# Performance work log

Measured on AMD Instinct MI355X. Metric: run time of the kernel, lower is better.

The kernel has to match this reference:

```python
import jax, jax.numpy as jnp
import numpy as np

B, Q, K, A, H, C, O = 32, 512, 512, 256, 8, 32, 256  # batch, queries, keys, channels, heads, head_dim, out_dim


def setup_inputs() -> dict:
    key = jax.random.key(0)
    ks = jax.random.split(key, 12)
    s = 0.02
    return {
        "q_data": jax.random.normal(ks[0], (B, Q, A), jnp.float32),
        "m_data": jax.random.normal(ks[1], (B, K, A), jnp.float32),
        "bias": jax.random.normal(ks[2], (B, 1, 1, K), jnp.float32),
        "nonbatched_bias": jax.random.normal(ks[3], (H, Q, K), jnp.float32),
        "batched_bias": jax.random.normal(ks[4], (B, H, Q, K), jnp.float32),
        "query_w": jax.random.normal(ks[5], (A, H, C), jnp.float32) * s,
        "key_w": jax.random.normal(ks[6], (A, H, C), jnp.float32) * s,
        "value_w": jax.random.normal(ks[7], (A, H, C), jnp.float32) * s,
        "gating_w": jax.random.normal(ks[8], (A, H, C), jnp.float32) * s,
        "gating_b": jnp.ones((H, C), jnp.float32),
        "output_w": jax.random.normal(ks[9], (H, C, O), jnp.float32) * s,
        "output_b": jnp.zeros((O,), jnp.float32),
    }


def reference(q_data, m_data, bias, nonbatched_bias, batched_bias,
              query_w, key_w, value_w, gating_w, gating_b, output_w, output_b):
    key_scale = query_w.shape[-1] ** -0.5
    q = jnp.einsum('bqa,ahc->bqhc', q_data, query_w) * key_scale
    k = jnp.einsum('bka,ahc->bkhc', m_data, key_w)
    v = jnp.einsum('bka,ahc->bkhc', m_data, value_w)
    logits = jnp.einsum('bqhc,bkhc->bhqk', q, k) + bias
    logits = logits + nonbatched_bias[None] + batched_bias
    weights = jax.nn.softmax(logits, axis=-1)
    weighted_avg = jnp.einsum('bhqk,bkhc->bqhc', weights, v)
    gate = jax.nn.sigmoid(jnp.einsum('bqc,chv->bqhv', q_data, gating_w) + gating_b)
    weighted_avg = weighted_avg * gate
    return jnp.einsum('bqhc,hco->bqo', weighted_avg, output_w) + output_b
```

## Files before the change

kernel.cpp:

```cpp
#include <hip/hip_runtime.h>
#include <cstdint>
#include <cstddef>


typedef __attribute__((ext_vector_type(8))) short short8;
typedef __attribute__((ext_vector_type(4))) float f32x4;
typedef __attribute__((ext_vector_type(4))) unsigned int u32x4;
typedef __attribute__((ext_vector_type(2))) unsigned int u32x2;

#define DEVFN static __device__ __forceinline__
#define L2E 1.4426950408889634f

DEVFN float b2f(unsigned int bits16) {
  return __builtin_bit_cast(float, bits16 << 16);
}
DEVFN unsigned int pack2(float a, float b) {
  unsigned int r;
  asm("v_cvt_pk_bf16_f32 %0, %1, %2" : "=v"(r) : "v"(a), "v"(b));
  return r;
}
DEVFN f32x4 mfma16(short8 a, short8 b, f32x4 c) {
  return __builtin_amdgcn_mfma_f32_16x16x32_bf16(a, b, c, 0, 0, 0);
}
#define GLOAD_LDS16(gp, lp)                                        \
  __builtin_amdgcn_global_load_lds(                                \
      (const __attribute__((address_space(1))) void*)(gp),         \
      (__attribute__((address_space(3))) void*)(lp), 16, 0, 0)

__global__ __launch_bounds__(256) void wtrans_kernel(
    const float* __restrict__ qw, const float* __restrict__ kw,
    const float* __restrict__ vw, const float* __restrict__ gw,
    const float* __restrict__ ow,
    unsigned short* __restrict__ wtq, unsigned short* __restrict__ wtk,
    unsigned short* __restrict__ wtv, unsigned short* __restrict__ wtg,
    unsigned short* __restrict__ wt3)
{
  const int matid = blockIdx.x >> 4;
  const int tile  = blockIdx.x & 15;
  const float* src = (matid == 0) ? qw : (matid == 1) ? kw : (matid == 2) ? vw
                   : (matid == 3) ? gw : ow;
  unsigned short* dst = (matid == 0) ? wtq : (matid == 1) ? wtk : (matid == 2) ? wtv
                      : (matid == 3) ? wtg : wt3;
  const int tr = (tile >> 2) * 64, tc = (tile & 3) * 64;
  __shared__ unsigned short T[64 * 72];
  const int t = threadIdx.x;
  {
    const int row = t >> 2, cb = (t & 3) * 16;
#pragma unroll
    for (int ii = 0; ii < 4; ++ii) {
      f32x4 v = *(const f32x4*)&src[(size_t)(tr + row) * 256 + tc + cb + ii * 4];
      u32x2 p; p.x = pack2(v.x, v.y); p.y = pack2(v.z, v.w);
      *(u32x2*)&T[row * 72 + cb + ii * 4] = p;
    }
  }
  __syncthreads();
  {
    const int c0 = t >> 2, rb = (t & 3) * 16;
    unsigned short vals[16];
#pragma unroll
    for (int m = 0; m < 16; ++m) vals[m] = T[(rb + m) * 72 + c0];
    u32x4 s0, s1;
    s0.x = (unsigned)vals[0]  | ((unsigned)vals[1]  << 16);
    s0.y = (unsigned)vals[2]  | ((unsigned)vals[3]  << 16);
    s0.z = (unsigned)vals[4]  | ((unsigned)vals[5]  << 16);
    s0.w = (unsigned)vals[6]  | ((unsigned)vals[7]  << 16);
    s1.x = (unsigned)vals[8]  | ((unsigned)vals[9]  << 16);
    s1.y = (unsigned)vals[10] | ((unsigned)vals[11] << 16);
    s1.z = (unsigned)vals[12] | ((unsigned)vals[13] << 16);
    s1.w = (unsigned)vals[14] | ((unsigned)vals[15] << 16);
    unsigned short* dp = &dst[(size_t)(tc + c0) * 256 + tr + rb];
    *(u32x4*)dp = s0;
    *(u32x4*)(dp + 8) = s1;
  }
}

__global__ __launch_bounds__(512, 4) void proj_kernel(
    const float* __restrict__ q_data, const float* __restrict__ m_data,
    const unsigned short* __restrict__ wtq, const unsigned short* __restrict__ wtk,
    const unsigned short* __restrict__ wtv, const unsigned short* __restrict__ wtg,
    const float* __restrict__ gating_b,
    unsigned short* __restrict__ qp, unsigned short* __restrict__ kp,
    unsigned short* __restrict__ vp, unsigned short* __restrict__ gate)
{
  const int bid = blockIdx.x;
  const bool mside = bid >= 256;
  const int r0 = (mside ? bid - 256 : bid) * 64;
  const float* inp = mside ? m_data : q_data;
  __shared__ unsigned short Alds[64 * 264];
  __shared__ unsigned short Wlds[2][256 * 40];
  const int t = threadIdx.x;
  const int lane = t & 63, wave = t >> 6;
  const int l15 = lane & 15, g = lane >> 4;
  const int stripe = wave & 3, nhalf = wave >> 2;

  {
    const int row = t >> 3, cb = (t & 7) * 32;
    const float* ip = &inp[(size_t)(r0 + row) * 256 + cb];
#pragma unroll
    for (int i = 0; i < 4; ++i) {
      f32x4 a0 = *(const f32x4*)&ip[i * 8];
      f32x4 a1 = *(const f32x4*)&ip[i * 8 + 4];
      u32x4 pk;
      pk.x = pack2(a0.x, a0.y); pk.y = pack2(a0.z, a0.w);
      pk.z = pack2(a1.x, a1.y); pk.w = pack2(a1.z, a1.w);
      *(u32x4*)&Alds[row * 264 + cb + i * 8] = pk;
    }
  }

  const unsigned short* wt0 = mside ? wtk : wtq;
  const unsigned short* wt1 = mside ? wtv : wtg;
  const int wrow = t & 255, whalf = t >> 8;

  {
    const u32x4* wsrc = (const u32x4*)&wt0[(size_t)wrow * 256 + whalf * 16];
    u32x4 a = wsrc[0], b = wsrc[1];
    *(u32x4*)&Wlds[0][wrow * 40 + whalf * 16 + 0] = a;
    *(u32x4*)&Wlds[0][wrow * 40 + whalf * 16 + 8] = b;
  }

  f32x4 acc[8];
#pragma unroll
  for (int j = 0; j < 8; ++j) acc[j] = f32x4{0.f, 0.f, 0.f, 0.f};

  const int arow = (stripe * 16 + l15) * 264 + 8 * g;
  const int grow = r0 + stripe * 16 + l15;
  const int ob = grow >> 9, oq = grow & 511;

#pragma unroll
  for (int s = 0; s < 16; ++s) {
    const int p = s & 1;
    __syncthreads();
    u32x4 nw0, nw1;
    if (s < 15) {
      const unsigned short* wt = (s + 1 < 8) ? wt0 : wt1;
      const u32x4* wsrc =
          (const u32x4*)&wt[(size_t)wrow * 256 + ((s + 1) & 7) * 32 + whalf * 16];
      nw0 = wsrc[0]; nw1 = wsrc[1];
    }
    const int ks = s & 7;
    short8 bf = __builtin_bit_cast(short8, *(const u32x4*)&Alds[arow + ks * 32]);
#pragma unroll
    for (int j = 0; j < 8; ++j) {
      short8 wf = __builtin_bit_cast(short8,
          *(const u32x4*)&Wlds[p][((nhalf * 8 + j) * 16 + l15) * 40 + 8 * g]);
      acc[j] = mfma16(wf, bf, acc[j]);
    }
    if (s < 15) {
      *(u32x4*)&Wlds[p ^ 1][wrow * 40 + whalf * 16 + 0] = nw0;
      *(u32x4*)&Wlds[p ^ 1][wrow * 40 + whalf * 16 + 8] = nw1;
    }
    if (s == 7 || s == 15) {
      const int oi = s >> 3;
      const float QS = 0.17677669529663687f * 1.4426950408889634f;
#pragma unroll
      for (int j = 0; j < 8; ++j) {
        const int n0 = (nhalf * 8 + j) * 16 + 4 * g;
        const int h = n0 >> 5, c0 = n0 & 31;
        const size_t idx = ((size_t)(ob * 8 + h) * 512 + oq) * 32 + c0;
        f32x4 v = acc[j];
        if (!mside) {
          if (oi == 0) {
            u32x2 st;
            st.x = pack2(v.x * QS, v.y * QS);
            st.y = pack2(v.z * QS, v.w * QS);
            *(u32x2*)&qp[idx] = st;
          } else {
            f32x4 gb = *(const f32x4*)&gating_b[n0];
            f32x4 gv;
            gv.x = 1.0f / (1.0f + exp2f(-(v.x + gb.x) * L2E));
            gv.y = 1.0f / (1.0f + exp2f(-(v.y + gb.y) * L2E));
            gv.z = 1.0f / (1.0f + exp2f(-(v.z + gb.z) * L2E));
            gv.w = 1.0f / (1.0f + exp2f(-(v.w + gb.w) * L2E));
            u32x2 st;
            st.x = pack2(gv.x, gv.y); st.y = pack2(gv.z, gv.w);
            *(u32x2*)&gate[idx] = st;
          }
        } else {
          u32x2 st;
          st.x = pack2(v.x, v.y); st.y = pack2(v.z, v.w);
          if (oi == 0) *(u32x2*)&kp[idx] = st;
          else         *(u32x2*)&vp[idx] = st;
        }
        acc[j] = f32x4{0.f, 0.f, 0.f, 0.f};
      }
    }
  }
}

__global__ __launch_bounds__(512, 2) void attn_kernel(
    const unsigned short* __restrict__ qp, const unsigned short* __restrict__ kp,
    const unsigned short* __restrict__ vp,
    const float* __restrict__ bias, const float* __restrict__ nbias,
    const float* __restrict__ bbias,
    unsigned short* __restrict__ wa)
{
  const int bid = blockIdx.x;
  const int h = bid & 7;
  const int qh = (bid >> 3) & 1;
  const int b = bid >> 4;
  const int bh = b * 8 + h;
  const int t = threadIdx.x;
  const int lane = t & 63, wave = t >> 6;
  const int l15 = lane & 15, g = lane >> 4;

  __shared__ unsigned short Klds[512 * 40];
  __shared__ unsigned short Vt[32 * 520];
  __shared__ float Bb[2][8192];
  __shared__ float Bk[512];

  {
    const int row = t;
    const u32x4* ks = (const u32x4*)&kp[((size_t)bh * 512 + row) * 32];
    u32x4 k0 = ks[0], k1 = ks[1], k2 = ks[2], k3 = ks[3];
    *(u32x4*)&Klds[row * 40 + 0]  = k0;
    *(u32x4*)&Klds[row * 40 + 8]  = k1;
    *(u32x4*)&Klds[row * 40 + 16] = k2;
    *(u32x4*)&Klds[row * 40 + 24] = k3;
    const u32x4* vs = (const u32x4*)&vp[((size_t)bh * 512 + row) * 32];
#pragma unroll
    for (int cc = 0; cc < 4; ++cc) {
      u32x4 vv = vs[cc];
      unsigned int dw0 = vv.x, dw1 = vv.y, dw2 = vv.z, dw3 = vv.w;
      const int c = cc * 8;
      Vt[(c + 0) * 520 + row] = (unsigned short)(dw0 & 0xffff);
      Vt[(c + 1) * 520 + row] = (unsigned short)(dw0 >> 16);
      Vt[(c + 2) * 520 + row] = (unsigned short)(dw1 & 0xffff);
      Vt[(c + 3) * 520 + row] = (unsigned short)(dw1 >> 16);
      Vt[(c + 4) * 520 + row] = (unsigned short)(dw2 & 0xffff);
      Vt[(c + 5) * 520 + row] = (unsigned short)(dw2 >> 16);
      Vt[(c + 6) * 520 + row] = (unsigned short)(dw3 & 0xffff);
      Vt[(c + 7) * 520 + row] = (unsigned short)(dw3 >> 16);
    }
    if (t < 128) {
      f32x4 bv = *(const f32x4*)&bias[(size_t)b * 512 + t * 4];
      bv.x *= L2E; bv.y *= L2E; bv.z *= L2E; bv.w *= L2E;
      *(f32x4*)&Bk[t * 4] = bv;
    }
  }

  const int qbase = qh * 256 + wave * 32;
  short8 qf[2];
#pragma unroll
  for (int qt = 0; qt < 2; ++qt)
    qf[qt] = __builtin_bit_cast(short8,
        *(const u32x4*)&qp[((size_t)bh * 512 + qbase + qt * 16 + l15) * 32 + 8 * g]);

  const float* bbb_blk = bbias + (size_t)bh * 262144 + (size_t)(qh * 256) * 512;
  const int qc = lane >> 3, sl = lane & 7;
  const float* wsrc0 = bbb_blk + (size_t)(wave * 32) * 512
                     + (size_t)qc * 512 + ((sl ^ qc) << 2);

  const float* n0p = nbias + (size_t)h * 262144 + (size_t)(qbase + l15) * 512 + 4 * g;
  const float* n1p = n0p + 16 * 512;

  f32x4 acc[2][2];
#pragma unroll
  for (int ct = 0; ct < 2; ++ct)
#pragma unroll
    for (int qt = 0; qt < 2; ++qt) acc[ct][qt] = f32x4{0.f, 0.f, 0.f, 0.f};
  float l_part[2] = {0.f, 0.f};

#pragma unroll
  for (int i = 0; i < 4; ++i)
    GLOAD_LDS16(wsrc0 + (size_t)i * 4096, &Bb[0][(wave * 4 + i) * 256]);
#pragma unroll
  for (int i = 0; i < 4; ++i)
    GLOAD_LDS16(wsrc0 + (size_t)i * 4096 + 32, &Bb[1][(wave * 4 + i) * 256]);
  f32x4 Cn00 = *(const f32x4*)(n0p);
  f32x4 Cn01 = *(const f32x4*)(n0p + 16);
  f32x4 Cn10 = *(const f32x4*)(n1p);
  f32x4 Cn11 = *(const f32x4*)(n1p + 16);

  __syncthreads();

  const int pib = ((g & 1) << 4) | ((g >> 1) << 3);
  const bool godd = (g & 1) != 0;
  const int sw0 = (g ^ (l15 & 7)) << 2;
  const int sw1 = ((g + 4) ^ (l15 & 7)) << 2;
  const int bq0 = (wave * 32 + l15) * 32;
  const int bq1 = bq0 + 16 * 32;

  for (int kt = 0; kt < 16; ++kt) {
    const int p = kt & 1;
    const int k0 = kt * 32;
    short8 kf0 = __builtin_bit_cast(short8, *(const u32x4*)&Klds[(k0 + l15) * 40 + 8 * g]);
    short8 kf1 = __builtin_bit_cast(short8, *(const u32x4*)&Klds[(k0 + 16 + l15) * 40 + 8 * g]);
    short8 vf0 = __builtin_bit_cast(short8, *(const u32x4*)&Vt[l15 * 520 + k0 + pib]);
    short8 vf1 = __builtin_bit_cast(short8, *(const u32x4*)&Vt[(16 + l15) * 520 + k0 + pib]);
    f32x4 bks0 = *(const f32x4*)&Bk[k0 + 4 * g];
    f32x4 bks1 = *(const f32x4*)&Bk[k0 + 16 + 4 * g];
    const float* bp = Bb[p];
    f32x4 bb00 = *(const f32x4*)&bp[bq0 + sw0];
    f32x4 bb01 = *(const f32x4*)&bp[bq0 + sw1];
    f32x4 bb10 = *(const f32x4*)&bp[bq1 + sw0];
    f32x4 bb11 = *(const f32x4*)&bp[bq1 + sw1];

#pragma unroll
    for (int qt = 0; qt < 2; ++qt) {
      f32x4 bb0 = qt ? bb10 : bb00;
      f32x4 bb1 = qt ? bb11 : bb01;
      f32x4 nb0 = qt ? Cn10 : Cn00;
      f32x4 nb1 = qt ? Cn11 : Cn01;
      f32x4 c0 = bb0 * L2E + (nb0 * L2E + bks0);
      f32x4 c1 = bb1 * L2E + (nb1 * L2E + bks1);
      f32x4 s0 = mfma16(kf0, qf[qt], c0);
      f32x4 s1 = mfma16(kf1, qf[qt], c1);
      f32x4 p0, p1;
      p0.x = exp2f(s0.x); p0.y = exp2f(s0.y);
      p0.z = exp2f(s0.z); p0.w = exp2f(s0.w);
      p1.x = exp2f(s1.x); p1.y = exp2f(s1.y);
      p1.z = exp2f(s1.z); p1.w = exp2f(s1.w);
      l_part[qt] += ((p0.x + p0.y) + (p0.z + p0.w)) +
                    ((p1.x + p1.y) + (p1.z + p1.w));
      unsigned int d0 = pack2(p0.x, p0.y), d1 = pack2(p0.z, p0.w);
      unsigned int e0 = pack2(p1.x, p1.y), e1 = pack2(p1.z, p1.w);
      unsigned int pd0 = __shfl_xor(d0, 16, 64), pd1 = __shfl_xor(d1, 16, 64);
      unsigned int pe0 = __shfl_xor(e0, 16, 64), pe1 = __shfl_xor(e1, 16, 64);
      u32x4 pfu;
      pfu.x = godd ? pe0 : d0;
      pfu.y = godd ? pe1 : d1;
      pfu.z = godd ? e0 : pd0;
      pfu.w = godd ? e1 : pd1;
      short8 pf = __builtin_bit_cast(short8, pfu);
      acc[0][qt] = mfma16(vf0, pf, acc[0][qt]);
      acc[1][qt] = mfma16(vf1, pf, acc[1][qt]);
    }

    asm volatile("" ::: "memory");
    if (kt < 14) {
      const float* ws = wsrc0 + (size_t)(kt + 2) * 32;
#pragma unroll
      for (int i = 0; i < 4; ++i)
        GLOAD_LDS16(ws + (size_t)i * 4096, &Bb[p][(wave * 4 + i) * 256]);
    }
    if (kt < 15) {
      Cn00 = *(const f32x4*)(n0p + k0 + 32);
      Cn01 = *(const f32x4*)(n0p + k0 + 48);
      Cn10 = *(const f32x4*)(n1p + k0 + 32);
      Cn11 = *(const f32x4*)(n1p + k0 + 48);
    }
    if (kt < 14)       asm volatile("s_waitcnt vmcnt(8)" ::: "memory");
    else if (kt == 14) asm volatile("s_waitcnt vmcnt(4)" ::: "memory");
  }

  unsigned short* wab = wa + (size_t)bh * 512 * 32;
#pragma unroll
  for (int qt = 0; qt < 2; ++qt) {
    float l = l_part[qt];
    l += __shfl_xor(l, 16, 64);
    l += __shfl_xor(l, 32, 64);
    const float rl = 1.0f / l;
    const int q = qbase + qt * 16 + l15;
#pragma unroll
    for (int ct = 0; ct < 2; ++ct) {
      f32x4 v = acc[ct][qt];
      u32x2 st;
      st.x = pack2(v.x * rl, v.y * rl);
      st.y = pack2(v.z * rl, v.w * rl);
      *(u32x2*)&wab[q * 32 + ct * 16 + 4 * g] = st;
    }
  }
}

__global__ __launch_bounds__(256, 2) void outp_kernel(
    const unsigned short* __restrict__ wa, const unsigned short* __restrict__ gate,
    const unsigned short* __restrict__ wt3, const float* __restrict__ out_b,
    float* __restrict__ out)
{
  const int r0 = blockIdx.x * 32;
  const int t = threadIdx.x;
  const int lane = t & 63, wave = t >> 6;
  const int l15 = lane & 15, g = lane >> 4;
  const int stripe = wave & 1, half = wave >> 1;
  __shared__ unsigned short Wlds[2][256 * 40];

  const int grow = r0 + stripe * 16 + l15;
  const int b = grow >> 9, q = grow & 511;

  {
    const u32x4* wsrc = (const u32x4*)&wt3[(size_t)t * 256];
    u32x4 a = wsrc[0], bb = wsrc[1], c = wsrc[2], d = wsrc[3];
    *(u32x4*)&Wlds[0][t * 40 + 0]  = a;
    *(u32x4*)&Wlds[0][t * 40 + 8]  = bb;
    *(u32x4*)&Wlds[0][t * 40 + 16] = c;
    *(u32x4*)&Wlds[0][t * 40 + 24] = d;
  }
  size_t aidx = ((size_t)(b * 8 + 0) * 512 + q) * 32 + 8 * g;
  u32x4 cwv = *(const u32x4*)&wa[aidx];
  u32x4 cgv = *(const u32x4*)&gate[aidx];

  f32x4 acc[8];
#pragma unroll
  for (int j = 0; j < 8; ++j) acc[j] = f32x4{0.f, 0.f, 0.f, 0.f};

#pragma unroll
  for (int s = 0; s < 8; ++s) {
    const int p = s & 1;
    __syncthreads();
    u32x4 nw0, nw1, nw2, nw3, nwv, ngv;
    if (s < 7) {
      const u32x4* wsrc = (const u32x4*)&wt3[(size_t)t * 256 + (s + 1) * 32];
      nw0 = wsrc[0]; nw1 = wsrc[1]; nw2 = wsrc[2]; nw3 = wsrc[3];
      const size_t na = ((size_t)(b * 8 + s + 1) * 512 + q) * 32 + 8 * g;
      nwv = *(const u32x4*)&wa[na];
      ngv = *(const u32x4*)&gate[na];
    }
    float f0 = b2f(cwv.x & 0xffff) * b2f(cgv.x & 0xffff);
    float f1 = b2f(cwv.x >> 16)    * b2f(cgv.x >> 16);
    float f2 = b2f(cwv.y & 0xffff) * b2f(cgv.y & 0xffff);
    float f3 = b2f(cwv.y >> 16)    * b2f(cgv.y >> 16);
    float f4 = b2f(cwv.z & 0xffff) * b2f(cgv.z & 0xffff);
    float f5 = b2f(cwv.z >> 16)    * b2f(cgv.z >> 16);
    float f6 = b2f(cwv.w & 0xffff) * b2f(cgv.w & 0xffff);
    float f7 = b2f(cwv.w >> 16)    * b2f(cgv.w >> 16);
    u32x4 au;
    au.x = pack2(f0, f1); au.y = pack2(f2, f3);
    au.z = pack2(f4, f5); au.w = pack2(f6, f7);
    short8 af = __builtin_bit_cast(short8, au);
#pragma unroll
    for (int j = 0; j < 8; ++j) {
      short8 wf = __builtin_bit_cast(short8,
          *(const u32x4*)&Wlds[p][((half * 8 + j) * 16 + l15) * 40 + 8 * g]);
      acc[j] = mfma16(wf, af, acc[j]);
    }
    if (s < 7) {
      *(u32x4*)&Wlds[p ^ 1][t * 40 + 0]  = nw0;
      *(u32x4*)&Wlds[p ^ 1][t * 40 + 8]  = nw1;
      *(u32x4*)&Wlds[p ^ 1][t * 40 + 16] = nw2;
      *(u32x4*)&Wlds[p ^ 1][t * 40 + 24] = nw3;
      cwv = nwv; cgv = ngv;
    }
  }
#pragma unroll
  for (int j = 0; j < 8; ++j) {
    const int o0 = (half * 8 + j) * 16 + 4 * g;
    f32x4 ob4 = *(const f32x4*)&out_b[o0];
    f32x4 v = acc[j] + ob4;
    *(f32x4*)&out[(size_t)grow * 256 + o0] = v;
  }
}

extern "C" void kernel_launch(void* const* d_in, const int* in_sizes, int n_in,
                              void* d_out, int out_size, void* d_ws, size_t ws_size,
                              hipStream_t stream)
{
  const float* q_data   = (const float*)d_in[0];
  const float* m_data   = (const float*)d_in[1];
  const float* bias     = (const float*)d_in[2];
  const float* nbb      = (const float*)d_in[3];
  const float* bbb      = (const float*)d_in[4];
  const float* query_w  = (const float*)d_in[5];
  const float* key_w    = (const float*)d_in[6];
  const float* value_w  = (const float*)d_in[7];
  const float* gating_w = (const float*)d_in[8];
  const float* gating_b = (const float*)d_in[9];
  const float* output_w = (const float*)d_in[10];
  const float* output_b = (const float*)d_in[11];
  float* out = (float*)d_out;

  const size_t QP_B   = (size_t)32 * 8 * 512 * 32 * 2;
  const size_t GATE_B = (size_t)32 * 8 * 512 * 32 * 2;
  const size_t WT_B   = (size_t)256 * 256 * 2;

  char* ws = (char*)d_ws;
  unsigned short* qp  = (unsigned short*)(ws);
  unsigned short* kp  = (unsigned short*)(ws + QP_B);
  unsigned short* vp  = (unsigned short*)(ws + 2 * QP_B);
  unsigned short* wab = (unsigned short*)(ws + 3 * QP_B);
  unsigned short* gat = (unsigned short*)(ws + 4 * QP_B);
  unsigned short* wtq = (unsigned short*)(ws + 4 * QP_B + GATE_B);
  unsigned short* wtk = (unsigned short*)(ws + 4 * QP_B + GATE_B + WT_B);
  unsigned short* wtv = (unsigned short*)(ws + 4 * QP_B + GATE_B + 2 * WT_B);
  unsigned short* wtg = (unsigned short*)(ws + 4 * QP_B + GATE_B + 3 * WT_B);
  unsigned short* wt3 = (unsigned short*)(ws + 4 * QP_B + GATE_B + 4 * WT_B);
  const size_t need = 4 * QP_B + GATE_B + 5 * WT_B;
  if (ws_size < need) return;

  hipLaunchKernelGGL(wtrans_kernel, dim3(80), dim3(256), 0, stream,
                     query_w, key_w, value_w, gating_w, output_w,
                     wtq, wtk, wtv, wtg, wt3);
  hipLaunchKernelGGL(proj_kernel, dim3(512), dim3(512), 0, stream,
                     q_data, m_data, wtq, wtk, wtv, wtg, gating_b,
                     qp, kp, vp, gat);
  hipLaunchKernelGGL(attn_kernel, dim3(512), dim3(512), 0, stream,
                     qp, kp, vp, bias, nbb, bbb, wab);
  hipLaunchKernelGGL(outp_kernel, dim3(512), dim3(256), 0, stream,
                     wab, gat, wt3, output_b, out);
}
```

Before: 122.3 us.

## Process both query halves per attention block, reusing staged K/V across passes

The attention kernel now launches one block per (batch, head) instead of two. Each block loops over both 256-query halves in a single 32-step pipeline, so K and V are staged into LDS once instead of twice. The batched-bias prefetch now crosses the pass boundary, the next nonbatched-bias tile is loaded into separate registers with an explicit LDS wait and a scheduling barrier, and the K LDS row padding is removed. In exchange the grid is halved, which lowers parallelism on a large GPU, and the unpadded K rows may cause LDS bank conflicts.

```diff
diff --git a/kernel.cpp b/kernel.cpp
--- a/kernel.cpp
+++ b/kernel.cpp
@@ -196,26 +196,36 @@
 {
   const int bid = blockIdx.x;
   const int h = bid & 7;
-  const int qh = (bid >> 3) & 1;
-  const int b = bid >> 4;
-  const int bh = b * 8 + h;
+  const int b = bid >> 3;
+  const int bh = bid;
   const int t = threadIdx.x;
   const int lane = t & 63, wave = t >> 6;
   const int l15 = lane & 15, g = lane >> 4;
 
-  __shared__ unsigned short Klds[512 * 40];
+  __shared__ unsigned short Klds[512 * 32];
   __shared__ unsigned short Vt[32 * 520];
   __shared__ float Bb[2][8192];
   __shared__ float Bk[512];
 
+  const float* bbb_bh = bbias + (size_t)bh * 262144;
+  const int qc = lane >> 3, sl = lane & 7;
+  const float* wsrc0 = bbb_bh + (size_t)(wave * 32 + qc) * 512 + ((sl ^ qc) << 2);
+
+#pragma unroll
+  for (int i = 0; i < 4; ++i)
+    GLOAD_LDS16(wsrc0 + i * 4096,      &Bb[0][(wave * 4 + i) * 256]);
+#pragma unroll
+  for (int i = 0; i < 4; ++i)
+    GLOAD_LDS16(wsrc0 + i * 4096 + 32, &Bb[1][(wave * 4 + i) * 256]);
+
   {
     const int row = t;
     const u32x4* ks = (const u32x4*)&kp[((size_t)bh * 512 + row) * 32];
     u32x4 k0 = ks[0], k1 = ks[1], k2 = ks[2], k3 = ks[3];
-    *(u32x4*)&Klds[row * 40 + 0]  = k0;
-    *(u32x4*)&Klds[row * 40 + 8]  = k1;
-    *(u32x4*)&Klds[row * 40 + 16] = k2;
-    *(u32x4*)&Klds[row * 40 + 24] = k3;
+    *(u32x4*)&Klds[row * 32 + 0]  = k0;
+    *(u32x4*)&Klds[row * 32 + 8]  = k1;
+    *(u32x4*)&Klds[row * 32 + 16] = k2;
+    *(u32x4*)&Klds[row * 32 + 24] = k3;
     const u32x4* vs = (const u32x4*)&vp[((size_t)bh * 512 + row) * 32];
 #pragma unroll
     for (int cc = 0; cc < 4; ++cc) {
@@ -238,41 +248,6 @@
     }
   }
 
-  const int qbase = qh * 256 + wave * 32;
-  short8 qf[2];
-#pragma unroll
-  for (int qt = 0; qt < 2; ++qt)
-    qf[qt] = __builtin_bit_cast(short8,
-        *(const u32x4*)&qp[((size_t)bh * 512 + qbase + qt * 16 + l15) * 32 + 8 * g]);
-
-  const float* bbb_blk = bbias + (size_t)bh * 262144 + (size_t)(qh * 256) * 512;
-  const int qc = lane >> 3, sl = lane & 7;
-  const float* wsrc0 = bbb_blk + (size_t)(wave * 32) * 512
-                     + (size_t)qc * 512 + ((sl ^ qc) << 2);
-
-  const float* n0p = nbias + (size_t)h * 262144 + (size_t)(qbase + l15) * 512 + 4 * g;
-  const float* n1p = n0p + 16 * 512;
-
-  f32x4 acc[2][2];
-#pragma unroll
-  for (int ct = 0; ct < 2; ++ct)
-#pragma unroll
-    for (int qt = 0; qt < 2; ++qt) acc[ct][qt] = f32x4{0.f, 0.f, 0.f, 0.f};
-  float l_part[2] = {0.f, 0.f};
-
-#pragma unroll
-  for (int i = 0; i < 4; ++i)
-    GLOAD_LDS16(wsrc0 + (size_t)i * 4096, &Bb[0][(wave * 4 + i) * 256]);
-#pragma unroll
-  for (int i = 0; i < 4; ++i)
-    GLOAD_LDS16(wsrc0 + (size_t)i * 4096 + 32, &Bb[1][(wave * 4 + i) * 256]);
-  f32x4 Cn00 = *(const f32x4*)(n0p);
-  f32x4 Cn01 = *(const f32x4*)(n0p + 16);
-  f32x4 Cn10 = *(const f32x4*)(n1p);
-  f32x4 Cn11 = *(const f32x4*)(n1p + 16);
-
-  __syncthreads();
-
   const int pib = ((g & 1) << 4) | ((g >> 1) << 3);
   const bool godd = (g & 1) != 0;
   const int sw0 = (g ^ (l15 & 7)) << 2;
@@ -280,11 +255,41 @@
   const int bq0 = (wave * 32 + l15) * 32;
   const int bq1 = bq0 + 16 * 32;
 
-  for (int kt = 0; kt < 16; ++kt) {
-    const int p = kt & 1;
+  f32x4 Cn00, Cn01, Cn10, Cn11;
+  {
+    const float* nn = nbias + (size_t)h * 262144
+                    + (size_t)(wave * 32 + l15) * 512 + 4 * g;
+    Cn00 = *(const f32x4*)nn;
+    Cn01 = *(const f32x4*)(nn + 16);
+    Cn10 = *(const f32x4*)(nn + 16 * 512);
+    Cn11 = *(const f32x4*)(nn + 16 * 512 + 16);
+  }
+
+  short8 qf0, qf1;
+  f32x4 acc[2][2];
+  float l_part[2] = {0.f, 0.f};
+
+  __syncthreads();
+
+  for (int tok = 0; tok < 32; ++tok) {
+    const int pass = tok >> 4, kt = tok & 15, p = tok & 1;
     const int k0 = kt * 32;
-    short8 kf0 = __builtin_bit_cast(short8, *(const u32x4*)&Klds[(k0 + l15) * 40 + 8 * g]);
-    short8 kf1 = __builtin_bit_cast(short8, *(const u32x4*)&Klds[(k0 + 16 + l15) * 40 + 8 * g]);
+
+    if (kt == 0) {
+      const int qbase = pass * 256 + wave * 32;
+      qf0 = __builtin_bit_cast(short8,
+          *(const u32x4*)&qp[((size_t)bh * 512 + qbase + l15) * 32 + 8 * g]);
+      qf1 = __builtin_bit_cast(short8,
+          *(const u32x4*)&qp[((size_t)bh * 512 + qbase + 16 + l15) * 32 + 8 * g]);
+#pragma unroll
+      for (int ct = 0; ct < 2; ++ct)
+#pragma unroll
+        for (int qt = 0; qt < 2; ++qt) acc[ct][qt] = f32x4{0.f, 0.f, 0.f, 0.f};
+      l_part[0] = 0.f; l_part[1] = 0.f;
+    }
+
+    short8 kf0 = __builtin_bit_cast(short8, *(const u32x4*)&Klds[(k0 + l15) * 32 + 8 * g]);
+    short8 kf1 = __builtin_bit_cast(short8, *(const u32x4*)&Klds[(k0 + 16 + l15) * 32 + 8 * g]);
     short8 vf0 = __builtin_bit_cast(short8, *(const u32x4*)&Vt[l15 * 520 + k0 + pib]);
     short8 vf1 = __builtin_bit_cast(short8, *(const u32x4*)&Vt[(16 + l15) * 520 + k0 + pib]);
     f32x4 bks0 = *(const f32x4*)&Bk[k0 + 4 * g];
@@ -294,6 +299,27 @@
     f32x4 bb01 = *(const f32x4*)&bp[bq0 + sw1];
     f32x4 bb10 = *(const f32x4*)&bp[bq1 + sw0];
     f32x4 bb11 = *(const f32x4*)&bp[bq1 + sw1];
+    asm volatile("s_waitcnt lgkmcnt(0)" ::: "memory");
+    __builtin_amdgcn_sched_barrier(0);
+
+    f32x4 Nn00, Nn01, Nn10, Nn11;
+    if (tok < 31) {
+      const int nt = tok + 1;
+      const float* nn = nbias + (size_t)h * 262144
+          + (size_t)((nt >> 4) * 256 + wave * 32 + l15) * 512 + (nt & 15) * 32 + 4 * g;
+      Nn00 = *(const f32x4*)nn;
+      Nn01 = *(const f32x4*)(nn + 16);
+      Nn10 = *(const f32x4*)(nn + 16 * 512);
+      Nn11 = *(const f32x4*)(nn + 16 * 512 + 16);
+    }
+
+    if (tok < 30) {
+      const int ft = tok + 2;
+      const float* ws = wsrc0 + (size_t)(ft >> 4) * 131072 + (ft & 15) * 32;
+#pragma unroll
+      for (int i = 0; i < 4; ++i)
+        GLOAD_LDS16(ws + (size_t)i * 4096, &Bb[p][(wave * 4 + i) * 256]);
+    }
 
 #pragma unroll
     for (int qt = 0; qt < 2; ++qt) {
@@ -303,8 +329,9 @@
       f32x4 nb1 = qt ? Cn11 : Cn01;
       f32x4 c0 = bb0 * L2E + (nb0 * L2E + bks0);
       f32x4 c1 = bb1 * L2E + (nb1 * L2E + bks1);
-      f32x4 s0 = mfma16(kf0, qf[qt], c0);
-      f32x4 s1 = mfma16(kf1, qf[qt], c1);
+      short8 qf = qt ? qf1 : qf0;
+      f32x4 s0 = mfma16(kf0, qf, c0);
+      f32x4 s1 = mfma16(kf1, qf, c1);
       f32x4 p0, p1;
       p0.x = exp2f(s0.x); p0.y = exp2f(s0.y);
       p0.z = exp2f(s0.z); p0.w = exp2f(s0.w);
@@ -326,38 +353,30 @@
       acc[1][qt] = mfma16(vf1, pf, acc[1][qt]);
     }
 
-    asm volatile("" ::: "memory");
-    if (kt < 14) {
-      const float* ws = wsrc0 + (size_t)(kt + 2) * 32;
-#pragma unroll
-      for (int i = 0; i < 4; ++i)
-        GLOAD_LDS16(ws + (size_t)i * 4096, &Bb[p][(wave * 4 + i) * 256]);
-    }
-    if (kt < 15) {
-      Cn00 = *(const f32x4*)(n0p + k0 + 32);
-      Cn01 = *(const f32x4*)(n0p + k0 + 48);
-      Cn10 = *(const f32x4*)(n1p + k0 + 32);
-      Cn11 = *(const f32x4*)(n1p + k0 + 48);
-    }
-    if (kt < 14)       asm volatile("s_waitcnt vmcnt(8)" ::: "memory");
-    else if (kt == 14) asm volatile("s_waitcnt vmcnt(4)" ::: "memory");
-  }
-
-  unsigned short* wab = wa + (size_t)bh * 512 * 32;
-#pragma unroll
-  for (int qt = 0; qt < 2; ++qt) {
-    float l = l_part[qt];
-    l += __shfl_xor(l, 16, 64);
-    l += __shfl_xor(l, 32, 64);
-    const float rl = 1.0f / l;
-    const int q = qbase + qt * 16 + l15;
-#pragma unroll
-    for (int ct = 0; ct < 2; ++ct) {
-      f32x4 v = acc[ct][qt];
-      u32x2 st;
-      st.x = pack2(v.x * rl, v.y * rl);
-      st.y = pack2(v.z * rl, v.w * rl);
-      *(u32x2*)&wab[q * 32 + ct * 16 + 4 * g] = st;
+    if (tok < 31) { Cn00 = Nn00; Cn01 = Nn01; Cn10 = Nn10; Cn11 = Nn11; }
+
+    if (tok < 30)       asm volatile("s_waitcnt vmcnt(8)" ::: "memory");
+    else if (tok == 30) asm volatile("s_waitcnt vmcnt(4)" ::: "memory");
+
+    if (kt == 15) {
+      const int qbase = pass * 256 + wave * 32;
+      unsigned short* wab = wa + (size_t)bh * 512 * 32;
+#pragma unroll
+      for (int qt = 0; qt < 2; ++qt) {
+        float l = l_part[qt];
+        l += __shfl_xor(l, 16, 64);
+        l += __shfl_xor(l, 32, 64);
+        const float rl = 1.0f / l;
+        const int q = qbase + qt * 16 + l15;
+#pragma unroll
+        for (int ct = 0; ct < 2; ++ct) {
+          f32x4 v = acc[ct][qt];
+          u32x2 st;
+          st.x = pack2(v.x * rl, v.y * rl);
+          st.y = pack2(v.z * rl, v.w * rl);
+          *(u32x2*)&wab[q * 32 + ct * 16 + 4 * g] = st;
+        }
+      }
     }
   }
 }
@@ -482,7 +501,7 @@
   hipLaunchKernelGGL(proj_kernel, dim3(512), dim3(512), 0, stream,
                      q_data, m_data, wtq, wtk, wtv, wtg, gating_b,
                      qp, kp, vp, gat);
-  hipLaunchKernelGGL(attn_kernel, dim3(512), dim3(512), 0, stream,
+  hipLaunchKernelGGL(attn_kernel, dim3(256), dim3(512), 0, stream,
                      qp, kp, vp, bias, nbb, bbb, wab);
   hipLaunchKernelGGL(outp_kernel, dim3(512), dim3(256), 0, stream,
                      wab, gat, wt3, output_b, out);
```

After: 122.2 us. About the same (-0.1%).
